# Optimization experiments

Measured on AMD Instinct MI355X. Metric: run time of the kernel, lower is better.

Reference implementation:

```python
import jax, jax.numpy as jnp
import numpy as np

N_HEADS = 32
N_KV_HEADS = 8
DIM = 4096
HEAD_DIM = DIM // N_HEADS  # 128
N_REP = N_HEADS // N_KV_HEADS  # 4
MAX_B = 4
CACHE_LEN = 1024
SEQ = 1024
BATCH = 4


def _rope(t, cos, sin):
    # t: (b, s, h, hd); interpret last dim as interleaved complex pairs
    tr = t[..., 0::2]
    ti = t[..., 1::2]
    cos = cos[None, :, None, :]
    sin = sin[None, :, None, :]
    out_r = tr * cos - ti * sin
    out_i = tr * sin + ti * cos
    return jnp.stack([out_r, out_i], axis=-1).reshape(t.shape)


def setup_inputs() -> dict:
    key = jax.random.key(0)
    ks = jax.random.split(key, 6)
    x = jax.random.normal(ks[0], (BATCH, SEQ, DIM), dtype=jnp.float32)
    wq = jax.random.normal(ks[1], (DIM, N_HEADS * HEAD_DIM), dtype=jnp.float32) * (DIM ** -0.5)
    wk = jax.random.normal(ks[2], (DIM, N_KV_HEADS * HEAD_DIM), dtype=jnp.float32) * (DIM ** -0.5)
    wv = jax.random.normal(ks[3], (DIM, N_KV_HEADS * HEAD_DIM), dtype=jnp.float32) * (DIM ** -0.5)
    wo = jax.random.normal(ks[4], (DIM, DIM), dtype=jnp.float32) * (DIM ** -0.5)
    # standard RoPE frequencies, theta = 10000
    inv_freq = 1.0 / (10000.0 ** (np.arange(0, HEAD_DIM, 2, dtype=np.float32) / HEAD_DIM))
    pos = np.arange(SEQ, dtype=np.float32)
    ang = np.outer(pos, inv_freq)  # (SEQ, HEAD_DIM/2)
    freqs_cos = jnp.asarray(np.cos(ang), dtype=jnp.float32)
    freqs_sin = jnp.asarray(np.sin(ang), dtype=jnp.float32)
    return {"x": x, "freqs_cos": freqs_cos, "freqs_sin": freqs_sin,
            "wq": wq, "wk": wk, "wv": wv, "wo": wo, "start": 0}


def reference(x, freqs_cos, freqs_sin, wq, wk, wv, wo, start):
    b, s, _ = x.shape
    xq = (x @ wq).reshape(b, s, N_HEADS, HEAD_DIM)
    xk = (x @ wk).reshape(b, s, N_KV_HEADS, HEAD_DIM)
    xv = (x @ wv).reshape(b, s, N_KV_HEADS, HEAD_DIM)

    xq = _rope(xq, freqs_cos, freqs_sin)
    xk = _rope(xk, freqs_cos, freqs_sin)

    # KV cache append (cache initialized to zeros as in the module)
    cache_k = jnp.zeros((MAX_B, CACHE_LEN, N_KV_HEADS, HEAD_DIM), dtype=x.dtype)
    cache_v = jnp.zeros((MAX_B, CACHE_LEN, N_KV_HEADS, HEAD_DIM), dtype=x.dtype)
    cache_k = cache_k.at[:b, start:start + s].set(xk)
    cache_v = cache_v.at[:b, start:start + s].set(xv)

    keys = cache_k[:b, :start + s]    # (b, kv, n_kv, hd)
    values = cache_v[:b, :start + s]

    # repeat_kv to match query heads (GQA)
    keys = jnp.repeat(keys, N_REP, axis=2)      # (b, kv, n_q, hd)
    values = jnp.repeat(values, N_REP, axis=2)

    scale = 1.0 / jnp.sqrt(jnp.float32(HEAD_DIM)).astype(x.dtype)
    scores = jnp.einsum('bqhd,bkhd->bhqk', xq, keys) * scale
    probs = jax.nn.softmax(scores, axis=-1)
    out = jnp.einsum('bhqk,bkhd->bqhd', probs, values).reshape(b, s, DIM)
    return out @ wo
```

## Files before the change

kernel.cpp:

```cpp
#include <hip/hip_runtime.h>
#include <cstdint>

#define B_SZ 4
#define S_LEN 1024
#define DIM 4096
#define NH 32
#define KVH 8
#define HD 128
#define DQKV 6144

typedef __bf16 bf16x8 __attribute__((ext_vector_type(8)));
typedef float f32x4 __attribute__((ext_vector_type(4)));

__device__ __forceinline__ unsigned short f2bf(float f) {
  union { float f; uint32_t u; } v; v.f = f;
  uint32_t u = v.u;
  return (unsigned short)((u + 0x7fffu + ((u >> 16) & 1u)) >> 16);
}
__device__ __forceinline__ float bf2f(unsigned short h) {
  union { uint32_t u; float f; } v; v.u = ((uint32_t)h) << 16;
  return v.f;
}
__device__ __forceinline__ float ex2(float x) {
#if __has_builtin(__builtin_amdgcn_exp2f)
  return __builtin_amdgcn_exp2f(x);
#else
  return exp2f(x);
#endif
}

__device__ __forceinline__ void async16(void* lds, const void* g) {
  __builtin_amdgcn_global_load_lds(
      (const __attribute__((address_space(1))) void*)g,
      (__attribute__((address_space(3))) void*)lds, 16, 0, 0);
}

__global__ void cvt_x_kernel(const float* __restrict__ x, unsigned short* __restrict__ xb) {
  size_t i = ((size_t)blockIdx.x * 256 + threadIdx.x) * 4;
  float4 v = *(const float4*)(x + i);
  ushort4 o;
  o.x = f2bf(v.x); o.y = f2bf(v.y); o.z = f2bf(v.z); o.w = f2bf(v.w);
  *(ushort4*)(xb + i) = o;
}

__global__ void wtrans_kernel(const float* __restrict__ w, unsigned short* __restrict__ wt, int N) {
  __shared__ float tile[64][65];
  int n0 = blockIdx.x * 64, k0 = blockIdx.y * 64;
  int tx = threadIdx.x & 63, ty = threadIdx.x >> 6;
#pragma unroll
  for (int i = 0; i < 16; i++) {
    int k = ty + i * 4;
    tile[k][tx] = w[(size_t)(k0 + k) * N + n0 + tx];
  }
  __syncthreads();
  int c = threadIdx.x & 31, ny = threadIdx.x >> 5;
#pragma unroll
  for (int i = 0; i < 8; i++) {
    int n = ny + i * 8;
    ushort2 o;
    o.x = f2bf(tile[2 * c][n]);
    o.y = f2bf(tile[2 * c + 1][n]);
    *(ushort2*)(wt + (size_t)(n0 + n) * DIM + k0 + 2 * c) = o;
  }
}

template <bool OUT_BF16>
__global__ __launch_bounds__(512, 2) void gemm256_kernel(
    const unsigned short* __restrict__ A, const unsigned short* __restrict__ Bt,
    void* __restrict__ Cout, int Kdim, int ldc) {
  __shared__ __align__(16) unsigned short sh[2 * 32768];
  const int tid = threadIdx.x;
  const int wave = tid >> 6, lane = tid & 63;
  const int nbx = gridDim.x;
  const int nb = nbx * (int)gridDim.y;
  const int bid = (int)blockIdx.y * nbx + (int)blockIdx.x;
  const int sb = (bid & 7) * (nb >> 3) + (bid >> 3);
  const int m0 = (sb / nbx) * 256, n0 = (sb % nbx) * 256;

  const int r0 = tid >> 3;
  const int cs0 = (tid & 7) ^ (r0 & 7);
  const unsigned short* gA = A + (size_t)(m0 + r0) * Kdim + cs0 * 8;
  const unsigned short* gB = Bt + (size_t)(n0 + r0) * Kdim + cs0 * 8;
  const size_t row64 = (size_t)64 * Kdim;
  const size_t row128 = (size_t)128 * Kdim;

  const int wm = wave >> 2, wn = wave & 3;
  const int rl = lane & 15, lh4 = lane >> 4;
  const int pc0 = (lh4 ^ (rl & 7)) * 8;
  const int pc1 = ((lh4 + 4) ^ (rl & 7)) * 8;
  const int arow = (wm * 128 + rl) * 64;
  const int brow = (wn * 64 + rl) * 64;

  f32x4 acc[8][4] = {};

#define STAGEH(BUF, AB, H, GS) do {                                               \
    unsigned short* d_ = sh + (BUF) * 32768 + (AB) * 16384 + (H) * 8192 + wave * 512; \
    async16(d_, (GS));                                                            \
    async16(d_ + 4096, (GS) + row64);                                             \
  } while (0)

#define PHASEQ(Q, STAGE_STMT, WAIT_STMT) do {                                     \
    af[0][0] = *(const bf16x8*)(bufA + arow + (2 * (Q)) * 1024 + pc0);            \
    af[0][1] = *(const bf16x8*)(bufA + arow + (2 * (Q)) * 1024 + pc1);            \
    af[1][0] = *(const bf16x8*)(bufA + arow + (2 * (Q) + 1) * 1024 + pc0);        \
    af[1][1] = *(const bf16x8*)(bufA + arow + (2 * (Q) + 1) * 1024 + pc1);        \
    STAGE_STMT;                                                                   \
    WAIT_STMT;                                                                    \
    __builtin_amdgcn_s_barrier();                                                 \
    __builtin_amdgcn_s_setprio(1);                                                \
    _Pragma("unroll") for (int i = 0; i < 2; i++)                                 \
      _Pragma("unroll") for (int n = 0; n < 4; n++) {                             \
        acc[2 * (Q) + i][n] = __builtin_amdgcn_mfma_f32_16x16x32_bf16(            \
            af[i][0], bf[n][0], acc[2 * (Q) + i][n], 0, 0, 0);                    \
        acc[2 * (Q) + i][n] = __builtin_amdgcn_mfma_f32_16x16x32_bf16(            \
            af[i][1], bf[n][1], acc[2 * (Q) + i][n], 0, 0, 0);                    \
      }                                                                           \
    __builtin_amdgcn_s_setprio(0);                                                \
    __builtin_amdgcn_s_barrier();                                                 \
  } while (0)

  const int NT = Kdim >> 6;
  STAGEH(0, 0, 0, gA);
  STAGEH(0, 0, 1, gA + row128);
  STAGEH(0, 1, 0, gB);
  STAGEH(0, 1, 1, gB + row128);
  STAGEH(1, 1, 0, gB + 64);
  STAGEH(1, 1, 1, gB + row128 + 64);
  asm volatile("s_waitcnt vmcnt(4)" ::: "memory");
  __builtin_amdgcn_s_barrier();

  for (int t = 0; t < NT; ++t) {
    const int cur = t & 1;
    const unsigned short* bufA = sh + cur * 32768;
    const unsigned short* bufB = bufA + 16384;
    bf16x8 bf[4][2];
    bf16x8 af[2][2];
#pragma unroll
    for (int n = 0; n < 4; n++) {
      bf[n][0] = *(const bf16x8*)(bufB + brow + n * 1024 + pc0);
      bf[n][1] = *(const bf16x8*)(bufB + brow + n * 1024 + pc1);
    }
    PHASEQ(0, if (t + 1 < NT) STAGEH(cur ^ 1, 0, 0, gA + (size_t)(t + 1) * 64), );
    PHASEQ(1, if (t + 1 < NT) STAGEH(cur ^ 1, 0, 1, gA + row128 + (size_t)(t + 1) * 64), );
    PHASEQ(2, if (t + 2 < NT) STAGEH(cur, 1, 0, gB + (size_t)(t + 2) * 64), );
    PHASEQ(3, if (t + 2 < NT) STAGEH(cur, 1, 1, gB + row128 + (size_t)(t + 2) * 64),
           if (t < NT - 2) { asm volatile("s_waitcnt vmcnt(4)" ::: "memory"); }
           else if (t == NT - 2) { asm volatile("s_waitcnt vmcnt(0)" ::: "memory"); });
  }
#undef STAGEH
#undef PHASEQ

#pragma unroll
  for (int m = 0; m < 8; m++)
#pragma unroll
    for (int n = 0; n < 4; n++)
#pragma unroll
      for (int reg = 0; reg < 4; reg++) {
        int row = m0 + wm * 128 + m * 16 + lh4 * 4 + reg;
        int col = n0 + wn * 64 + n * 16 + rl;
        float v = acc[m][n][reg];
        if (OUT_BF16)
          ((unsigned short*)Cout)[(size_t)row * ldc + col] = f2bf(v);
        else
          ((float*)Cout)[(size_t)row * ldc + col] = v;
      }
}

__global__ void rope_kernel(const unsigned short* __restrict__ src, const float* __restrict__ fc,
                            const float* __restrict__ fs, unsigned short* __restrict__ dst,
                            int nheads, int hshift, float scale) {
  int idx = blockIdx.x * 256 + threadIdx.x;
  int f4 = idx & 15;
  int rest = idx >> 4;
  int hh = rest & (nheads - 1);
  int t = rest >> hshift;
  int s = t & (S_LEN - 1);
  int b = t >> 10;
  union { uint4 v; unsigned short u[8]; } in, out;
  in.v = *(const uint4*)(src + (size_t)t * DQKV + hh * HD + f4 * 8);
  union { float4 v; float f[4]; } c4, s4;
  c4.v = *(const float4*)(fc + s * 64 + f4 * 4);
  s4.v = *(const float4*)(fs + s * 64 + f4 * 4);
#pragma unroll
  for (int j = 0; j < 4; j++) {
    float xr = bf2f(in.u[2 * j]), xi = bf2f(in.u[2 * j + 1]);
    float cc = c4.f[j], ss = s4.f[j];
    out.u[2 * j] = f2bf((xr * cc - xi * ss) * scale);
    out.u[2 * j + 1] = f2bf((xr * ss + xi * cc) * scale);
  }
  *(uint4*)(dst + ((size_t)(b * nheads + hh) * S_LEN + s) * HD + f4 * 8) = out.v;
}

__global__ void vtrans_kernel(const unsigned short* __restrict__ src, unsigned short* __restrict__ Vt) {
  __shared__ __align__(16) unsigned short tile[32][33];
  int s0 = blockIdx.x * 32, d0 = blockIdx.y * 32, bk = blockIdx.z;
  int tx = threadIdx.x & 31, ty = threadIdx.x >> 5;
#pragma unroll
  for (int i = 0; i < 4; i++) {
    int s = ty + i * 8;
    tile[s][tx] = src[(size_t)((bk >> 3) * S_LEN + s0 + s) * DQKV + (bk & 7) * HD + d0 + tx];
  }
  __syncthreads();
#pragma unroll
  for (int i = 0; i < 4; i++) {
    int d = ty + i * 8;
    Vt[((size_t)bk * HD + d0 + d) * S_LEN + s0 + tx] = tile[tx][d];
  }
}

__global__ __launch_bounds__(256, 3) void attn_kernel(
    const unsigned short* __restrict__ Qb,
    const unsigned short* __restrict__ Kb,
    const unsigned short* __restrict__ Vt,
    unsigned short* __restrict__ Ob) {
  __shared__ __align__(16) unsigned short Kt[64][128];
  __shared__ __align__(16) unsigned short Vl[128][64];
  __shared__ __align__(16) unsigned short Pl[4][16][72];
  const int tid = threadIdx.x, wave = tid >> 6, lane = tid & 63;
  const int qb = blockIdx.x, h = blockIdx.y, b = blockIdx.z;
  const int kvh = h >> 2;
  const int lql = lane & 15, lqh = lane >> 4;
  const int qrow = qb * 64 + wave * 16;

  const unsigned short* Qp = Qb + ((size_t)(b * NH + h) * S_LEN + qrow + lql) * HD + lqh * 8;
  bf16x8 qf[4];
#pragma unroll
  for (int kd = 0; kd < 4; kd++) qf[kd] = *(const bf16x8*)(Qp + kd * 32);

  const unsigned short* Kp = Kb + (size_t)(b * KVH + kvh) * S_LEN * HD;
  const unsigned short* Vp = Vt + (size_t)(b * KVH + kvh) * HD * S_LEN;
  const int krow_in = lane >> 4;
  const int kcol_sw = lane & 15;
  const int vrow_in = lane >> 3;
  const int vcol_off = ((lane & 7) ^ (lane >> 3)) * 8;

  float m_run[4], l_run[4];
  f32x4 Oacc[8] = {};
#pragma unroll
  for (int r = 0; r < 4; r++) { m_run[r] = -3.0e38f; l_run[r] = 0.0f; }

  for (int kt = 0; kt < S_LEN; kt += 64) {
    __syncthreads();
#pragma unroll
    for (int j = 0; j < 4; j++) {
      int rbase = wave * 16 + j * 4;
      int r = rbase + krow_in;
      async16(&Kt[rbase][0], Kp + (size_t)(kt + r) * HD + ((kcol_sw ^ (r & 7)) * 8));
    }
#pragma unroll
    for (int j = 0; j < 4; j++) {
      int dbase = wave * 32 + j * 8;
      int d = dbase + vrow_in;
      async16(&Vl[dbase][0], Vp + (size_t)d * S_LEN + kt + vcol_off);
    }
    __syncthreads();
    f32x4 sf[4] = {};
#pragma unroll
    for (int ni = 0; ni < 4; ni++) {
      const int ksw = lql & 7;
#pragma unroll
      for (int kd = 0; kd < 4; kd++) {
        bf16x8 kf = *(const bf16x8*)(&Kt[ni * 16 + lql][((kd * 4 + lqh) ^ ksw) * 8]);
        sf[ni] = __builtin_amdgcn_mfma_f32_16x16x32_bf16(qf[kd], kf, sf[ni], 0, 0, 0);
      }
    }
    float mnew[4], alpha[4], psum[4];
#pragma unroll
    for (int r = 0; r < 4; r++) {
      float v = fmaxf(fmaxf(sf[0][r], sf[1][r]), fmaxf(sf[2][r], sf[3][r]));
      v = fmaxf(v, __shfl_xor(v, 1));
      v = fmaxf(v, __shfl_xor(v, 2));
      v = fmaxf(v, __shfl_xor(v, 4));
      v = fmaxf(v, __shfl_xor(v, 8));
      mnew[r] = fmaxf(m_run[r], v);
      alpha[r] = ex2(m_run[r] - mnew[r]);
      m_run[r] = mnew[r];
      psum[r] = 0.0f;
    }
#pragma unroll
    for (int ni = 0; ni < 4; ni++)
#pragma unroll
      for (int r = 0; r < 4; r++) {
        float p = ex2(sf[ni][r] - mnew[r]);
        psum[r] += p;
        union { float f; uint32_t u; } pv; pv.f = p;
        Pl[wave][lqh * 4 + r][ni * 16 + lql] = (unsigned short)(pv.u >> 16);
      }
#pragma unroll
    for (int r = 0; r < 4; r++) {
      float v = psum[r];
      v += __shfl_xor(v, 1);
      v += __shfl_xor(v, 2);
      v += __shfl_xor(v, 4);
      v += __shfl_xor(v, 8);
      l_run[r] = l_run[r] * alpha[r] + v;
    }
#pragma unroll
    for (int ni = 0; ni < 8; ni++)
#pragma unroll
      for (int r = 0; r < 4; r++) Oacc[ni][r] *= alpha[r];
    bf16x8 pa[2];
#pragma unroll
    for (int ks = 0; ks < 2; ks++)
      pa[ks] = *(const bf16x8*)(&Pl[wave][lql][ks * 32 + lqh * 8]);
#pragma unroll
    for (int ni = 0; ni < 8; ni++) {
      const int ksw = lql & 7;
#pragma unroll
      for (int ks = 0; ks < 2; ks++) {
        bf16x8 vb = *(const bf16x8*)(&Vl[ni * 16 + lql][((ks * 4 + lqh) ^ ksw) * 8]);
        Oacc[ni] = __builtin_amdgcn_mfma_f32_16x16x32_bf16(pa[ks], vb, Oacc[ni], 0, 0, 0);
      }
    }
  }
#pragma unroll
  for (int r = 0; r < 4; r++) l_run[r] = 1.0f / l_run[r];
#pragma unroll
  for (int ni = 0; ni < 8; ni++)
#pragma unroll
    for (int r = 0; r < 4; r++) {
      int q = qrow + lqh * 4 + r;
      Ob[(size_t)(b * S_LEN + q) * DIM + h * HD + ni * 16 + lql] = f2bf(Oacc[ni][r] * l_run[r]);
    }
}

extern "C" void kernel_launch(void* const* d_in, const int* in_sizes, int n_in,
                              void* d_out, int out_size, void* d_ws, size_t ws_size,
                              hipStream_t stream) {
  (void)in_sizes; (void)n_in; (void)out_size; (void)ws_size;
  const float* x  = (const float*)d_in[0];
  const float* fc = (const float*)d_in[1];
  const float* fs = (const float*)d_in[2];
  const float* wq = (const float*)d_in[3];
  const float* wk = (const float*)d_in[4];
  const float* wv = (const float*)d_in[5];
  const float* wo = (const float*)d_in[6];
  float* out = (float*)d_out;
  char* ws = (char*)d_ws;

  const size_t MB = 1024 * 1024;
  unsigned short* xb    = (unsigned short*)(ws + 0);
  unsigned short* attnb = (unsigned short*)(ws + 0);
  unsigned short* wqkvt = (unsigned short*)(ws + 32 * MB);
  unsigned short* Qb    = (unsigned short*)(ws + 32 * MB);
  unsigned short* Kb    = (unsigned short*)(ws + 64 * MB);
  unsigned short* Vt    = (unsigned short*)(ws + 72 * MB);
  unsigned short* wot   = (unsigned short*)(ws + 80 * MB);
  unsigned short* qkv   = (unsigned short*)(ws + 112 * MB);

  cvt_x_kernel<<<16384, 256, 0, stream>>>(x, xb);
  wtrans_kernel<<<dim3(64, 64), 256, 0, stream>>>(wq, wqkvt, 4096);
  wtrans_kernel<<<dim3(16, 64), 256, 0, stream>>>(wk, wqkvt + (size_t)4096 * 4096, 1024);
  wtrans_kernel<<<dim3(16, 64), 256, 0, stream>>>(wv, wqkvt + (size_t)5120 * 4096, 1024);
  wtrans_kernel<<<dim3(64, 64), 256, 0, stream>>>(wo, wot, 4096);
  gemm256_kernel<true><<<dim3(DQKV / 256, 16), 512, 0, stream>>>(xb, wqkvt, qkv, DIM, DQKV);
  rope_kernel<<<8192, 256, 0, stream>>>(qkv, fc, fs, Qb, NH, 5, 0.12751879505099168f);
  rope_kernel<<<2048, 256, 0, stream>>>(qkv + 4096, fc, fs, Kb, KVH, 3, 1.0f);
  vtrans_kernel<<<dim3(32, 4, 32), 256, 0, stream>>>(qkv + 5120, Vt);
  attn_kernel<<<dim3(16, NH, B_SZ), 256, 0, stream>>>(Qb, Kb, Vt, attnb);
  gemm256_kernel<false><<<dim3(16, 16), 512, 0, stream>>>(attnb, wot, out, DIM, DIM);
}
```

Measured before the change: 760.3 us.

## Restructure GEMM LDS layout into K-half slabs with finer-grained prefetch schedule

```diff
diff --git a/kernel.cpp b/kernel.cpp
--- a/kernel.cpp
+++ b/kernel.cpp
@@ -77,78 +77,76 @@
   const int sb = (bid & 7) * (nb >> 3) + (bid >> 3);
   const int m0 = (sb / nbx) * 256, n0 = (sb % nbx) * 256;
 
-  const int r0 = tid >> 3;
-  const int cs0 = (tid & 7) ^ (r0 & 7);
-  const unsigned short* gA = A + (size_t)(m0 + r0) * Kdim + cs0 * 8;
-  const unsigned short* gB = Bt + (size_t)(n0 + r0) * Kdim + cs0 * 8;
-  const size_t row64 = (size_t)64 * Kdim;
+  const int r0 = tid >> 2;
+  const int cs = (tid & 3) ^ ((tid >> 3) & 3);
+  const unsigned short* gA = A + (size_t)(m0 + r0) * Kdim + cs * 8;
+  const unsigned short* gB = Bt + (size_t)(n0 + r0) * Kdim + cs * 8;
   const size_t row128 = (size_t)128 * Kdim;
 
   const int wm = wave >> 2, wn = wave & 3;
   const int rl = lane & 15, lh4 = lane >> 4;
-  const int pc0 = (lh4 ^ (rl & 7)) * 8;
-  const int pc1 = ((lh4 + 4) ^ (rl & 7)) * 8;
-  const int arow = (wm * 128 + rl) * 64;
-  const int brow = (wn * 64 + rl) * 64;
+  const int pc = (lh4 ^ ((rl >> 1) & 3)) * 8;
+  const int arow = (wm * 128 + rl) * 32 + pc;
+  const int brow = (wn * 64 + rl) * 32 + pc;
 
   f32x4 acc[8][4] = {};
-
-#define STAGEH(BUF, AB, H, GS) do {                                               \
-    unsigned short* d_ = sh + (BUF) * 32768 + (AB) * 16384 + (H) * 8192 + wave * 512; \
-    async16(d_, (GS));                                                            \
-    async16(d_ + 4096, (GS) + row64);                                             \
+  bf16x8 af[4], bf[4];
+
+#define STG(BUF, BASEL, GPTR, KOFF) do {                                   \
+    unsigned short* d_ = sh + (BUF) * 32768 + (BASEL) + wave * 512;        \
+    async16(d_, (GPTR) + (KOFF));                                          \
+    async16(d_ + 4096, (GPTR) + row128 + (KOFF));                          \
   } while (0)
 
-#define PHASEQ(Q, STAGE_STMT, WAIT_STMT) do {                                     \
-    af[0][0] = *(const bf16x8*)(bufA + arow + (2 * (Q)) * 1024 + pc0);            \
-    af[0][1] = *(const bf16x8*)(bufA + arow + (2 * (Q)) * 1024 + pc1);            \
-    af[1][0] = *(const bf16x8*)(bufA + arow + (2 * (Q) + 1) * 1024 + pc0);        \
-    af[1][1] = *(const bf16x8*)(bufA + arow + (2 * (Q) + 1) * 1024 + pc1);        \
-    STAGE_STMT;                                                                   \
-    WAIT_STMT;                                                                    \
-    __builtin_amdgcn_s_barrier();                                                 \
-    __builtin_amdgcn_s_setprio(1);                                                \
-    _Pragma("unroll") for (int i = 0; i < 2; i++)                                 \
-      _Pragma("unroll") for (int n = 0; n < 4; n++) {                             \
-        acc[2 * (Q) + i][n] = __builtin_amdgcn_mfma_f32_16x16x32_bf16(            \
-            af[i][0], bf[n][0], acc[2 * (Q) + i][n], 0, 0, 0);                    \
-        acc[2 * (Q) + i][n] = __builtin_amdgcn_mfma_f32_16x16x32_bf16(            \
-            af[i][1], bf[n][1], acc[2 * (Q) + i][n], 0, 0, 0);                    \
-      }                                                                           \
-    __builtin_amdgcn_s_setprio(0);                                                \
-    __builtin_amdgcn_s_barrier();                                                 \
+#define PH(MH, KH, READB, STAGE_STMT, WAIT_STMT) do {                      \
+    const unsigned short* bA_ = buf + (KH) * 8192;                         \
+    _Pragma("unroll") for (int i = 0; i < 4; i++)                          \
+      af[i] = *(const bf16x8*)(bA_ + arow + ((MH) * 4 + i) * 512);         \
+    if (READB) {                                                           \
+      const unsigned short* bB_ = buf + 16384 + (KH) * 8192;               \
+      _Pragma("unroll") for (int n = 0; n < 4; n++)                        \
+        bf[n] = *(const bf16x8*)(bB_ + brow + n * 512);                    \
+    }                                                                      \
+    STAGE_STMT;                                                            \
+    WAIT_STMT;                                                             \
+    __builtin_amdgcn_s_barrier();                                          \
+    __builtin_amdgcn_s_setprio(1);                                         \
+    _Pragma("unroll") for (int i = 0; i < 4; i++)                          \
+      _Pragma("unroll") for (int n = 0; n < 4; n++)                        \
+        acc[(MH) * 4 + i][n] = __builtin_amdgcn_mfma_f32_16x16x32_bf16(    \
+            af[i], bf[n], acc[(MH) * 4 + i][n], 0, 0, 0);                  \
+    __builtin_amdgcn_s_setprio(0);                                         \
+    __builtin_amdgcn_s_barrier();                                          \
   } while (0)
 
   const int NT = Kdim >> 6;
-  STAGEH(0, 0, 0, gA);
-  STAGEH(0, 0, 1, gA + row128);
-  STAGEH(0, 1, 0, gB);
-  STAGEH(0, 1, 1, gB + row128);
-  STAGEH(1, 1, 0, gB + 64);
-  STAGEH(1, 1, 1, gB + row128 + 64);
+  STG(0, 0, gA, 0);
+  STG(0, 8192, gA, 32);
+  STG(0, 16384, gB, 0);
+  STG(0, 24576, gB, 32);
+  STG(1, 0, gA, 64);
+  STG(1, 16384, gB, 64);
   asm volatile("s_waitcnt vmcnt(4)" ::: "memory");
   __builtin_amdgcn_s_barrier();
 
   for (int t = 0; t < NT; ++t) {
-    const int cur = t & 1;
-    const unsigned short* bufA = sh + cur * 32768;
-    const unsigned short* bufB = bufA + 16384;
-    bf16x8 bf[4][2];
-    bf16x8 af[2][2];
-#pragma unroll
-    for (int n = 0; n < 4; n++) {
-      bf[n][0] = *(const bf16x8*)(bufB + brow + n * 1024 + pc0);
-      bf[n][1] = *(const bf16x8*)(bufB + brow + n * 1024 + pc1);
-    }
-    PHASEQ(0, if (t + 1 < NT) STAGEH(cur ^ 1, 0, 0, gA + (size_t)(t + 1) * 64), );
-    PHASEQ(1, if (t + 1 < NT) STAGEH(cur ^ 1, 0, 1, gA + row128 + (size_t)(t + 1) * 64), );
-    PHASEQ(2, if (t + 2 < NT) STAGEH(cur, 1, 0, gB + (size_t)(t + 2) * 64), );
-    PHASEQ(3, if (t + 2 < NT) STAGEH(cur, 1, 1, gB + row128 + (size_t)(t + 2) * 64),
-           if (t < NT - 2) { asm volatile("s_waitcnt vmcnt(4)" ::: "memory"); }
-           else if (t == NT - 2) { asm volatile("s_waitcnt vmcnt(0)" ::: "memory"); });
-  }
-#undef STAGEH
-#undef PHASEQ
+    const unsigned short* buf = sh + (t & 1) * 32768;
+    const int nbuf = (t & 1) ^ 1;
+    const size_t kb = (size_t)t * 64;
+    PH(0, 0, 1,
+       if (t + 1 < NT) { STG(nbuf, 8192, gA, kb + 96); STG(nbuf, 24576, gB, kb + 96); },
+       if (t + 1 < NT) { asm volatile("s_waitcnt vmcnt(8)" ::: "memory"); }
+       else { asm volatile("s_waitcnt vmcnt(0)" ::: "memory"); });
+    PH(1, 0, 0, , );
+    PH(0, 1, 1,
+       if (t + 2 < NT) { STG(t & 1, 0, gA, kb + 128); }, );
+    PH(1, 1, 0,
+       if (t + 2 < NT) { STG(t & 1, 16384, gB, kb + 128); },
+       if (t + 2 < NT) { asm volatile("s_waitcnt vmcnt(8)" ::: "memory"); }
+       else if (t + 1 < NT) { asm volatile("s_waitcnt vmcnt(4)" ::: "memory"); });
+  }
+#undef STG
+#undef PH
 
 #pragma unroll
   for (int m = 0; m < 8; m++)
```

Result: no change. 772.5 us (+1.6%).

## Load K and V MFMA fragments directly from global memory, dropping LDS staging

Applied to the files above, without the earlier changes.

```diff
diff --git a/kernel.cpp b/kernel.cpp
--- a/kernel.cpp
+++ b/kernel.cpp
@@ -213,8 +213,6 @@
     const unsigned short* __restrict__ Kb,
     const unsigned short* __restrict__ Vt,
     unsigned short* __restrict__ Ob) {
-  __shared__ __align__(16) unsigned short Kt[64][128];
-  __shared__ __align__(16) unsigned short Vl[128][64];
   __shared__ __align__(16) unsigned short Pl[4][16][72];
   const int tid = threadIdx.x, wave = tid >> 6, lane = tid & 63;
   const int qb = blockIdx.x, h = blockIdx.y, b = blockIdx.z;
@@ -227,12 +225,8 @@
 #pragma unroll
   for (int kd = 0; kd < 4; kd++) qf[kd] = *(const bf16x8*)(Qp + kd * 32);
 
-  const unsigned short* Kp = Kb + (size_t)(b * KVH + kvh) * S_LEN * HD;
-  const unsigned short* Vp = Vt + (size_t)(b * KVH + kvh) * HD * S_LEN;
-  const int krow_in = lane >> 4;
-  const int kcol_sw = lane & 15;
-  const int vrow_in = lane >> 3;
-  const int vcol_off = ((lane & 7) ^ (lane >> 3)) * 8;
+  const unsigned short* Kp = Kb + (size_t)(b * KVH + kvh) * S_LEN * HD + (size_t)lql * HD + lqh * 8;
+  const unsigned short* Vp = Vt + (size_t)(b * KVH + kvh) * HD * S_LEN + (size_t)lql * S_LEN + lqh * 8;
 
   float m_run[4], l_run[4];
   f32x4 Oacc[8] = {};
@@ -240,27 +234,12 @@
   for (int r = 0; r < 4; r++) { m_run[r] = -3.0e38f; l_run[r] = 0.0f; }
 
   for (int kt = 0; kt < S_LEN; kt += 64) {
-    __syncthreads();
-#pragma unroll
-    for (int j = 0; j < 4; j++) {
-      int rbase = wave * 16 + j * 4;
-      int r = rbase + krow_in;
-      async16(&Kt[rbase][0], Kp + (size_t)(kt + r) * HD + ((kcol_sw ^ (r & 7)) * 8));
-    }
-#pragma unroll
-    for (int j = 0; j < 4; j++) {
-      int dbase = wave * 32 + j * 8;
-      int d = dbase + vrow_in;
-      async16(&Vl[dbase][0], Vp + (size_t)d * S_LEN + kt + vcol_off);
-    }
-    __syncthreads();
     f32x4 sf[4] = {};
 #pragma unroll
     for (int ni = 0; ni < 4; ni++) {
-      const int ksw = lql & 7;
 #pragma unroll
       for (int kd = 0; kd < 4; kd++) {
-        bf16x8 kf = *(const bf16x8*)(&Kt[ni * 16 + lql][((kd * 4 + lqh) ^ ksw) * 8]);
+        bf16x8 kf = *(const bf16x8*)(Kp + (size_t)(kt + ni * 16) * HD + kd * 32);
         sf[ni] = __builtin_amdgcn_mfma_f32_16x16x32_bf16(qf[kd], kf, sf[ni], 0, 0, 0);
       }
     }
@@ -305,10 +284,9 @@
       pa[ks] = *(const bf16x8*)(&Pl[wave][lql][ks * 32 + lqh * 8]);
 #pragma unroll
     for (int ni = 0; ni < 8; ni++) {
-      const int ksw = lql & 7;
 #pragma unroll
       for (int ks = 0; ks < 2; ks++) {
-        bf16x8 vb = *(const bf16x8*)(&Vl[ni * 16 + lql][((ks * 4 + lqh) ^ ksw) * 8]);
+        bf16x8 vb = *(const bf16x8*)(Vp + (size_t)(ni * 16) * S_LEN + kt + ks * 32);
         Oacc[ni] = __builtin_amdgcn_mfma_f32_16x16x32_bf16(pa[ks], vb, Oacc[ni], 0, 0, 0);
       }
     }
```

New measurement: 1.124 ms. 1.48x slower.
